# Kernel tuning notes

Measured on AMD Instinct MI355X. Metric: run time of the kernel, lower is better.

## Reference

```python
import jax, jax.numpy as jnp
import numpy as np

NUM_HEADS = 16
D_MODEL = 1024
ROPE_THETA = 10000.0


def rope_cos_sin(H, W, head_dim, theta):
    # SAM2/SAM3 axial RoPE: first half of complex dims encode x, second half y.
    n = H * W
    t = jnp.arange(n)
    tx = (t % W).astype(jnp.float32)
    ty = (t // W).astype(jnp.float32)
    # freqs: 1 / theta^(arange(0, dim, 4)[:dim//4] / dim)
    exps = jnp.arange(0, head_dim, 4)[: head_dim // 4].astype(jnp.float32) / head_dim
    freqs = 1.0 / (theta ** exps)  # (head_dim//4,)
    ang = jnp.concatenate([tx[:, None] * freqs, ty[:, None] * freqs], axis=-1)  # (N, head_dim//2)
    return jnp.cos(ang), jnp.sin(ang)


def apply_rope(x, cos, sin):
    # x: (B, nh, N, D); pairs of features treated as complex numbers
    B, nh, N, D = x.shape
    xr = x.reshape(B, nh, N, D // 2, 2)
    xe, xo = xr[..., 0], xr[..., 1]
    oe = xe * cos - xo * sin
    oo = xe * sin + xo * cos
    return jnp.stack([oe, oo], axis=-1).reshape(B, nh, N, D)


def setup_inputs() -> dict:
    key = jax.random.key(0)
    ks = jax.random.split(key, 12)
    C = D_MODEL
    s = 1.0 / np.sqrt(C)
    inp = {
        "q": jax.random.normal(ks[0], (2, 2048, C), dtype=jnp.float32),
        "k": jax.random.normal(ks[1], (2, 2112, C), dtype=jnp.float32),
        "v": jax.random.normal(ks[2], (2, 2112, C), dtype=jnp.float32),
        "Wq": jax.random.normal(ks[3], (C, C), dtype=jnp.float32) * s,
        "bq": jax.random.normal(ks[4], (C,), dtype=jnp.float32) * s,
        "Wk": jax.random.normal(ks[5], (C, C), dtype=jnp.float32) * s,
        "bk": jax.random.normal(ks[6], (C,), dtype=jnp.float32) * s,
        "Wv": jax.random.normal(ks[7], (C, C), dtype=jnp.float32) * s,
        "bv": jax.random.normal(ks[8], (C,), dtype=jnp.float32) * s,
        "Wo": jax.random.normal(ks[9], (C, C), dtype=jnp.float32) * s,
        "bo": jax.random.normal(ks[10], (C,), dtype=jnp.float32) * s,
        "q_h": 32,
        "q_w": 64,
        "num_final_k_to_exclude": 64,
    }
    return inp


def reference(q, k, v, Wq, bq, Wk, bk, Wv, bv, Wo, bo, q_h, q_w, num_final_k_to_exclude):
    B, Nq, C = q.shape
    Nk = k.shape[1]
    nh = NUM_HEADS
    d = C // nh
    # QKV projections -> (B, nh, N, d)
    qh = (q @ Wq + bq).reshape(B, Nq, nh, d).transpose(0, 2, 1, 3)
    kh = (k @ Wk + bk).reshape(B, Nk, nh, d).transpose(0, 2, 1, 3)
    vh = (v @ Wv + bv).reshape(B, Nk, nh, d).transpose(0, 2, 1, 3)
    # RoPE on q and on first num_k_keep keys (exclude trailing pointer tokens)
    n_keep = Nk - num_final_k_to_exclude  # == q_h * q_w == Nq here
    cos, sin = rope_cos_sin(q_h, q_w, d, ROPE_THETA)
    qh = apply_rope(qh, cos, sin)
    k_rot = apply_rope(kh[:, :, :n_keep], cos, sin)
    kh = jnp.concatenate([k_rot, kh[:, :, n_keep:]], axis=2)
    # scaled dot-product attention
    scale = 1.0 / np.sqrt(d)
    scores = jnp.einsum("bhqd,bhkd->bhqk", qh, kh) * scale
    probs = jax.nn.softmax(scores, axis=-1)
    attn = jnp.einsum("bhqk,bhkd->bhqd", probs, vh)
    out = attn.transpose(0, 2, 1, 3).reshape(B, Nq, C)
    return out @ Wo + bo
```

## Files before the change

### kernel.cpp

```cpp
#include <hip/hip_runtime.h>

#define B_ 2
#define NQ 2048
#define NK 2112
#define CD 1024
#define NH 16
#define HD 64

typedef unsigned short u16;
typedef unsigned int u32;
typedef __attribute__((ext_vector_type(8))) __bf16 bf16x8;
typedef __attribute__((ext_vector_type(4))) float f32x4;

#define GPTR(p) ((const __attribute__((address_space(1))) void*)(p))
#define LPTR(p) ((__attribute__((address_space(3))) void*)(p))
#define GLL16(g, l) __builtin_amdgcn_global_load_lds(GPTR(g), LPTR(l), 16, 0, 0)

__device__ __forceinline__ u16 f2bf(float f) {
  u32 u = __float_as_uint(f);
  u32 r = u + 0x7fffu + ((u >> 16) & 1u);
  return (u16)(r >> 16);
}
__device__ __forceinline__ u32 pack2bf(float x, float y) {
  u32 a = __float_as_uint(x); a += 0x7fffu + ((a >> 16) & 1u);
  u32 b = __float_as_uint(y); b += 0x7fffu + ((b >> 16) & 1u);
  return __builtin_amdgcn_perm(b, a, 0x07060302u);
}

#define SC 0.18033688011112042f
#define NEGL2T 0.8304820237f
#define FSTEP 0.5623413252f

__global__ void prep_kernel(const float* __restrict__ q, const float* __restrict__ k,
                            const float* __restrict__ v, u16* __restrict__ qb,
                            u16* __restrict__ kb, u16* __restrict__ vb,
                            const float* __restrict__ W0, const float* __restrict__ W1,
                            const float* __restrict__ W2, const float* __restrict__ W3,
                            u16* __restrict__ T0, u16* __restrict__ T1,
                            u16* __restrict__ T2, u16* __restrict__ T3) {
  __shared__ u16 tile[32][33];
  int y = blockIdx.y;
  int t = threadIdx.x;
  if (y < 3) {
    const float* src = (y == 0) ? q : (y == 1) ? k : v;
    u16* dst = (y == 0) ? qb : (y == 1) ? kb : vb;
    int n4 = (y == 0) ? (B_ * NQ * CD / 4) : (B_ * NK * CD / 4);
    int i = blockIdx.x * 256 + t;
    if (i >= n4) return;
    float4 vv = ((const float4*)src)[i];
    ushort4 o;
    o.x = f2bf(vv.x); o.y = f2bf(vv.y); o.z = f2bf(vv.z); o.w = f2bf(vv.w);
    ((ushort4*)dst)[i] = o;
  } else {
    int x = blockIdx.x;
    if (x >= 4096) return;
    int which = x >> 10, xy = x & 1023;
    const float* src = (which == 0) ? W0 : (which == 1) ? W1 : (which == 2) ? W2 : W3;
    u16* dst = (which == 0) ? T0 : (which == 1) ? T1 : (which == 2) ? T2 : T3;
    int r0 = (xy >> 5) * 32, c0 = (xy & 31) * 32;
    int row = t >> 3, c4 = (t & 7) * 4;
    float4 vv = *(const float4*)&src[(r0 + row) * 1024 + c0 + c4];
    tile[row][c4 + 0] = f2bf(vv.x);
    tile[row][c4 + 1] = f2bf(vv.y);
    tile[row][c4 + 2] = f2bf(vv.z);
    tile[row][c4 + 3] = f2bf(vv.w);
    __syncthreads();
    ushort4 o;
    o.x = tile[c4 + 0][row];
    o.y = tile[c4 + 1][row];
    o.z = tile[c4 + 2][row];
    o.w = tile[c4 + 3][row];
    *(ushort4*)&dst[(c0 + row) * 1024 + r0 + c4] = o;
  }
}

__global__ __launch_bounds__(256, 2) void gemm_qkv(
    const u16* __restrict__ qb, const u16* __restrict__ kb, const u16* __restrict__ vb,
    const u16* __restrict__ wqt, const u16* __restrict__ wkt, const u16* __restrict__ wvt,
    const float* __restrict__ bq, const float* __restrict__ bk, const float* __restrict__ bv,
    u16* __restrict__ Qh, u16* __restrict__ Kh, u16* __restrict__ Vt) {
  __shared__ u16 As[2][128 * 32];
  __shared__ u16 Bs[2][128 * 32];
  const int z = blockIdx.z;
  if (z == 0 && blockIdx.y >= 32) return;
  const u16* A = (z == 0) ? qb : (z == 1) ? kb : vb;
  const u16* Bt = (z == 0) ? wqt : (z == 1) ? wkt : wvt;
  const float* bias = (z == 0) ? bq : (z == 1) ? bk : bv;
  const int BR = (z == 0) ? NQ : NK;

  const int t = threadIdx.x;
  const int lane = t & 63, w = t >> 6;
  const int lc = lane & 15, lq = lane >> 4;
  const int m0 = blockIdx.y * 128, n0 = blockIdx.x * 128;
  const int wm = (w >> 1) * 64, wn = (w & 1) * 64;
  f32x4 acc[4][4] = {};
  const u16* ga = A + (m0 + (t >> 2)) * 1024 + (t & 3) * 8;
  const u16* gb = Bt + (n0 + (t >> 2)) * 1024 + (t & 3) * 8;
  char* lA0 = (char*)&As[0][0] + w * 1024;
  char* lA1 = (char*)&As[1][0] + w * 1024;
  char* lB0 = (char*)&Bs[0][0] + w * 1024;
  char* lB1 = (char*)&Bs[1][0] + w * 1024;
  const bool swap = (z < 2);
  for (int k0 = 0; k0 < 1024; k0 += 64) {
    if (k0) __syncthreads();
    GLL16(ga + k0, lA0);
    GLL16(ga + 64 * 1024 + k0, lA0 + 4096);
    GLL16(ga + k0 + 32, lA1);
    GLL16(ga + 64 * 1024 + k0 + 32, lA1 + 4096);
    GLL16(gb + k0, lB0);
    GLL16(gb + 64 * 1024 + k0, lB0 + 4096);
    GLL16(gb + k0 + 32, lB1);
    GLL16(gb + 64 * 1024 + k0 + 32, lB1 + 4096);
    __syncthreads();
#pragma unroll
    for (int kk = 0; kk < 2; ++kk) {
      bf16x8 af[4], bf[4];
#pragma unroll
      for (int i = 0; i < 4; ++i) {
        af[i] = *(const bf16x8*)&As[kk][(wm + i * 16 + lc) * 32 + lq * 8];
        bf[i] = *(const bf16x8*)&Bs[kk][(wn + i * 16 + lc) * 32 + lq * 8];
      }
      if (swap) {
#pragma unroll
        for (int mi = 0; mi < 4; ++mi)
#pragma unroll
          for (int ni = 0; ni < 4; ++ni)
            acc[mi][ni] = __builtin_amdgcn_mfma_f32_16x16x32_bf16(bf[ni], af[mi], acc[mi][ni], 0, 0, 0);
      } else {
#pragma unroll
        for (int mi = 0; mi < 4; ++mi)
#pragma unroll
          for (int ni = 0; ni < 4; ++ni)
            acc[mi][ni] = __builtin_amdgcn_mfma_f32_16x16x32_bf16(af[mi], bf[ni], acc[mi][ni], 0, 0, 0);
      }
    }
  }

  if (swap) {
    u16* Out = (z == 0) ? Qh : Kh;
    const bool isQ = (z == 0);
#pragma unroll
    for (int ni = 0; ni < 4; ++ni) {
      int cb = n0 + wn + ni * 16 + lq * 4;
      float4 bv4 = *(const float4*)&bias[cb];
      int jj = (ni * 8 + lq * 2) & 15;
      bool jl = ni < 2;
      float f0 = exp2f((float)jj * -NEGL2T);
      float f1 = f0 * FSTEP;
#pragma unroll
      for (int mi = 0; mi < 4; ++mi) {
        int row = m0 + wm + mi * 16 + lc;
        int bb = row >= BR ? 1 : 0;
        int tok = row - bb * BR;
        float v0 = acc[mi][ni][0] + bv4.x;
        float v1 = acc[mi][ni][1] + bv4.y;
        float v2 = acc[mi][ni][2] + bv4.z;
        float v3 = acc[mi][ni][3] + bv4.w;
        uint2 pk;
        if (isQ || tok < 2048) {
          float pos = jl ? (float)(tok & 63) : (float)(tok >> 6);
          float s0, c0, s1, c1;
          __sincosf(pos * f0, &s0, &c0);
          __sincosf(pos * f1, &s1, &c1);
          float o0 = v0 * c0 - v1 * s0, o1 = v0 * s0 + v1 * c0;
          float o2 = v2 * c1 - v3 * s1, o3 = v2 * s1 + v3 * c1;
          if (isQ) { o0 *= SC; o1 *= SC; o2 *= SC; o3 *= SC; }
          pk.x = pack2bf(o0, o1);
          pk.y = pack2bf(o2, o3);
        } else {
          pk.x = pack2bf(v0, v1);
          pk.y = pack2bf(v2, v3);
        }
        *(uint2*)&Out[row * 1024 + cb] = pk;
      }
    }
  } else {
#pragma unroll
    for (int ni = 0; ni < 4; ++ni) {
      int col = n0 + wn + ni * 16 + lc;
      float bv = bias[col];
      int hh = col >> 6, dd = col & 63;
#pragma unroll
      for (int mi = 0; mi < 4; ++mi) {
        int row0 = m0 + wm + mi * 16 + lq * 4;
        int bb = row0 >= NK ? 1 : 0;
        int tok0 = row0 - bb * NK;
        uint2 pk;
        pk.x = pack2bf(acc[mi][ni][0] + bv, acc[mi][ni][1] + bv);
        pk.y = pack2bf(acc[mi][ni][2] + bv, acc[mi][ni][3] + bv);
        *(uint2*)&Vt[((bb * NH + hh) * HD + dd) * NK + tok0] = pk;
      }
    }
  }
}

__global__ __launch_bounds__(256, 2) void gemm_o(const u16* __restrict__ A,
                                                 const u16* __restrict__ Bt,
                                                 const float* __restrict__ bias,
                                                 float* __restrict__ Cout) {
  __shared__ u16 As[2][128 * 32];
  __shared__ u16 Bs[2][64 * 32];
  const int t = threadIdx.x;
  const int lane = t & 63, w = t >> 6;
  const int lc = lane & 15, lq = lane >> 4;
  const int m0 = blockIdx.y * 128, n0 = blockIdx.x * 64;
  const int wm = (w >> 1) * 64, wn = (w & 1) * 32;
  f32x4 acc[4][2] = {};
  const u16* ga = A + (m0 + (t >> 2)) * 1024 + (t & 3) * 8;
  const u16* gb = Bt + (n0 + (t >> 2)) * 1024 + (t & 3) * 8;
  char* lA0 = (char*)&As[0][0] + w * 1024;
  char* lA1 = (char*)&As[1][0] + w * 1024;
  char* lB0 = (char*)&Bs[0][0] + w * 1024;
  char* lB1 = (char*)&Bs[1][0] + w * 1024;
  for (int k0 = 0; k0 < 1024; k0 += 64) {
    if (k0) __syncthreads();
    GLL16(ga + k0, lA0);
    GLL16(ga + 64 * 1024 + k0, lA0 + 4096);
    GLL16(ga + k0 + 32, lA1);
    GLL16(ga + 64 * 1024 + k0 + 32, lA1 + 4096);
    GLL16(gb + k0, lB0);
    GLL16(gb + k0 + 32, lB1);
    __syncthreads();
#pragma unroll
    for (int kk = 0; kk < 2; ++kk) {
      bf16x8 af[4], bf[2];
#pragma unroll
      for (int i = 0; i < 4; ++i)
        af[i] = *(const bf16x8*)&As[kk][(wm + i * 16 + lc) * 32 + lq * 8];
#pragma unroll
      for (int i = 0; i < 2; ++i)
        bf[i] = *(const bf16x8*)&Bs[kk][(wn + i * 16 + lc) * 32 + lq * 8];
#pragma unroll
      for (int mi = 0; mi < 4; ++mi)
#pragma unroll
        for (int ni = 0; ni < 2; ++ni)
          acc[mi][ni] = __builtin_amdgcn_mfma_f32_16x16x32_bf16(bf[ni], af[mi], acc[mi][ni], 0, 0, 0);
    }
  }
#pragma unroll
  for (int ni = 0; ni < 2; ++ni) {
    int cb = n0 + wn + ni * 16 + lq * 4;
    float4 bv4 = *(const float4*)&bias[cb];
#pragma unroll
    for (int mi = 0; mi < 4; ++mi) {
      int row = m0 + wm + mi * 16 + lc;
      float4 o;
      o.x = acc[mi][ni][0] + bv4.x;
      o.y = acc[mi][ni][1] + bv4.y;
      o.z = acc[mi][ni][2] + bv4.z;
      o.w = acc[mi][ni][3] + bv4.w;
      *(float4*)&Cout[row * 1024 + cb] = o;
    }
  }
}

#define LSTR 72
__global__ __launch_bounds__(256, 2) void attn_kernel(const u16* __restrict__ Qh,
                                                      const u16* __restrict__ Kh,
                                                      const u16* __restrict__ Vt,
                                                      u16* __restrict__ AO) {
  __shared__ u16 QPs[128 * LSTR];
  __shared__ u16 Ks[2 * 64 * LSTR];
  __shared__ u16 Vs[2 * 64 * LSTR];
  const int t = threadIdx.x;
  const int lane = t & 63, w = t >> 6;
  const int lc = lane & 15, lq = lane >> 4;
  const int rr = lane >> 3, s = lane & 7;
  const int qt = blockIdx.x, h = blockIdx.y, b = blockIdx.z;

  {
    const u16* gq = Qh + (b * NQ + qt * 128 + w * 32 + rr) * CD + h * HD + s * 8;
    u16* lqp = &QPs[(w * 32 + rr) * LSTR + s * 8];
#pragma unroll
    for (int i = 0; i < 4; ++i)
      *(uint4*)(lqp + i * 8 * LSTR) = *(const uint4*)(gq + i * 8 * CD);
  }
  bf16x8 qf[2][2];
#pragma unroll
  for (int ni = 0; ni < 2; ++ni)
#pragma unroll
    for (int kk = 0; kk < 2; ++kk)
      qf[ni][kk] = *(const bf16x8*)&QPs[(w * 32 + ni * 16 + lc) * LSTR + kk * 32 + lq * 8];

  bf16x8 ones;
  {
    u32* op = (u32*)&ones;
    op[0] = op[1] = op[2] = op[3] = 0x3F803F80u;
  }

  const u16* gK = Kh + (b * NK + w * 16 + rr) * CD + h * HD + s * 8;
  const u16* gV = Vt + ((b * NH + h) * HD + w * 16 + rr) * NK + s * 8;
  const int sk0 = (w * 16 + rr) * LSTR + s * 8;
  const int sk1 = (w * 16 + 8 + rr) * LSTR + s * 8;

  uint4 kreg0 = *(const uint4*)(gK);
  uint4 kreg1 = *(const uint4*)(gK + 8 * CD);
  uint4 vreg0 = *(const uint4*)(gV);
  uint4 vreg1 = *(const uint4*)(gV + 8 * NK);
  *(uint4*)&Ks[sk0] = kreg0;
  *(uint4*)&Ks[sk1] = kreg1;
  *(uint4*)&Vs[sk0] = vreg0;
  *(uint4*)&Vs[sk1] = vreg1;
  kreg0 = *(const uint4*)(gK + 64 * CD);
  kreg1 = *(const uint4*)(gK + 64 * CD + 8 * CD);
  vreg0 = *(const uint4*)(gV + 64);
  vreg1 = *(const uint4*)(gV + 8 * NK + 64);
  __syncthreads();

  f32x4 oacc[2][4] = {};
  f32x4 lacc[2] = {};
  int p = 0;

  for (int j0 = 0; j0 < NK; j0 += 64) {
    const u16* Kc = &Ks[p * 64 * LSTR];

    f32x4 st[2][4] = {};
#pragma unroll
    for (int mi = 0; mi < 4; ++mi) {
      bf16x8 k0f = *(const bf16x8*)&Kc[(mi * 16 + lc) * LSTR + lq * 8];
      bf16x8 k1f = *(const bf16x8*)&Kc[(mi * 16 + lc) * LSTR + 32 + lq * 8];
#pragma unroll
      for (int ni = 0; ni < 2; ++ni) {
        st[ni][mi] = __builtin_amdgcn_mfma_f32_16x16x32_bf16(k0f, qf[ni][0], st[ni][mi], 0, 0, 0);
        st[ni][mi] = __builtin_amdgcn_mfma_f32_16x16x32_bf16(k1f, qf[ni][1], st[ni][mi], 0, 0, 0);
      }
    }
#pragma unroll
    for (int ni = 0; ni < 2; ++ni)
#pragma unroll
      for (int mi = 0; mi < 4; ++mi) {
        u32 e0 = __float_as_uint(__builtin_amdgcn_exp2f(st[ni][mi][0]));
        u32 e1 = __float_as_uint(__builtin_amdgcn_exp2f(st[ni][mi][1]));
        u32 e2 = __float_as_uint(__builtin_amdgcn_exp2f(st[ni][mi][2]));
        u32 e3 = __float_as_uint(__builtin_amdgcn_exp2f(st[ni][mi][3]));
        uint2 pk;
        pk.x = __builtin_amdgcn_perm(e1 + 0x8000u, e0 + 0x8000u, 0x07060302u);
        pk.y = __builtin_amdgcn_perm(e3 + 0x8000u, e2 + 0x8000u, 0x07060302u);
        *(uint2*)&QPs[(w * 32 + ni * 16 + lc) * LSTR + mi * 16 + lq * 4] = pk;
      }
#pragma unroll
    for (int kc = 0; kc < 2; ++kc) {
      bf16x8 pf[2], vf[4];
#pragma unroll
      for (int ni = 0; ni < 2; ++ni)
        pf[ni] = *(const bf16x8*)&QPs[(w * 32 + ni * 16 + lc) * LSTR + kc * 32 + lq * 8];
#pragma unroll
      for (int di = 0; di < 4; ++di)
        vf[di] = *(const bf16x8*)&Vs[p * 64 * LSTR + (di * 16 + lc) * LSTR + kc * 32 + lq * 8];
#pragma unroll
      for (int ni = 0; ni < 2; ++ni) {
#pragma unroll
        for (int di = 0; di < 4; ++di)
          oacc[ni][di] = __builtin_amdgcn_mfma_f32_16x16x32_bf16(pf[ni], vf[di], oacc[ni][di], 0, 0, 0);
        lacc[ni] = __builtin_amdgcn_mfma_f32_16x16x32_bf16(pf[ni], ones, lacc[ni], 0, 0, 0);
      }
    }

    if (j0 + 64 < NK) {
      u16* Kn = &Ks[(p ^ 1) * 64 * LSTR];
      u16* Vn = &Vs[(p ^ 1) * 64 * LSTR];
      *(uint4*)&Kn[sk0] = kreg0;
      *(uint4*)&Kn[sk1] = kreg1;
      *(uint4*)&Vn[sk0] = vreg0;
      *(uint4*)&Vn[sk1] = vreg1;
      if (j0 + 128 < NK) {
        kreg0 = *(const uint4*)(gK + (j0 + 128) * CD);
        kreg1 = *(const uint4*)(gK + (j0 + 128) * CD + 8 * CD);
        vreg0 = *(const uint4*)(gV + j0 + 128);
        vreg1 = *(const uint4*)(gV + 8 * NK + j0 + 128);
      }
    }
    __syncthreads();
    p ^= 1;
  }
#pragma unroll
  for (int ni = 0; ni < 2; ++ni)
#pragma unroll
    for (int r = 0; r < 4; ++r) {
      float inv = 1.0f / lacc[ni][r];
#pragma unroll
      for (int di = 0; di < 4; ++di) {
        int row = qt * 128 + w * 32 + ni * 16 + lq * 4 + r;
        int col = h * HD + di * 16 + lc;
        AO[(b * NQ + row) * CD + col] = f2bf(oacc[ni][di][r] * inv);
      }
    }
}

extern "C" void kernel_launch(void* const* d_in, const int* in_sizes, int n_in,
                              void* d_out, int out_size, void* d_ws, size_t ws_size,
                              hipStream_t stream) {
  const float* q  = (const float*)d_in[0];
  const float* k  = (const float*)d_in[1];
  const float* v  = (const float*)d_in[2];
  const float* Wq = (const float*)d_in[3];
  const float* bq = (const float*)d_in[4];
  const float* Wk = (const float*)d_in[5];
  const float* bk = (const float*)d_in[6];
  const float* Wv = (const float*)d_in[7];
  const float* bv = (const float*)d_in[8];
  const float* Wo = (const float*)d_in[9];
  const float* bo = (const float*)d_in[10];

  char* ws = (char*)d_ws;
  size_t off = 0;
  auto alloc = [&](size_t bytes) {
    char* p = ws + off;
    off += (bytes + 255) & ~(size_t)255;
    return p;
  };
  u16* qb  = (u16*)alloc((size_t)B_ * NQ * CD * 2);
  u16* kb  = (u16*)alloc((size_t)B_ * NK * CD * 2);
  u16* vb  = (u16*)alloc((size_t)B_ * NK * CD * 2);
  u16* wqt = (u16*)alloc((size_t)CD * CD * 2);
  u16* wkt = (u16*)alloc((size_t)CD * CD * 2);
  u16* wvt = (u16*)alloc((size_t)CD * CD * 2);
  u16* wot = (u16*)alloc((size_t)CD * CD * 2);
  u16* Qh  = (u16*)alloc((size_t)B_ * NQ * CD * 2);
  u16* Kh  = (u16*)alloc((size_t)B_ * NK * CD * 2);
  u16* Vt  = (u16*)alloc((size_t)B_ * NK * CD * 2);
  u16* AO  = (u16*)alloc((size_t)B_ * NQ * CD * 2);

  prep_kernel<<<dim3(4224, 4), 256, 0, stream>>>(q, k, v, qb, kb, vb,
                                                 Wq, Wk, Wv, Wo, wqt, wkt, wvt, wot);
  gemm_qkv<<<dim3(8, 33, 3), 256, 0, stream>>>(qb, kb, vb, wqt, wkt, wvt, bq, bk, bv, Qh, Kh, Vt);
  attn_kernel<<<dim3(16, NH, B_), 256, 0, stream>>>(Qh, Kh, Vt, AO);
  gemm_o<<<dim3(16, 32), 256, 0, stream>>>(AO, wot, bo, (float*)d_out);
}
```

Baseline: 246.6 us.

## Use 8 waves per attention block and reshape output GEMM tiles

```diff
diff --git a/kernel.cpp b/kernel.cpp
--- a/kernel.cpp
+++ b/kernel.cpp
@@ -194,18 +194,18 @@
   }
 }
 
-__global__ __launch_bounds__(256, 2) void gemm_o(const u16* __restrict__ A,
+__global__ __launch_bounds__(256, 4) void gemm_o(const u16* __restrict__ A,
                                                  const u16* __restrict__ Bt,
                                                  const float* __restrict__ bias,
                                                  float* __restrict__ Cout) {
-  __shared__ u16 As[2][128 * 32];
-  __shared__ u16 Bs[2][64 * 32];
+  __shared__ u16 As[2][64 * 32];
+  __shared__ u16 Bs[2][128 * 32];
   const int t = threadIdx.x;
   const int lane = t & 63, w = t >> 6;
   const int lc = lane & 15, lq = lane >> 4;
-  const int m0 = blockIdx.y * 128, n0 = blockIdx.x * 64;
-  const int wm = (w >> 1) * 64, wn = (w & 1) * 32;
-  f32x4 acc[4][2] = {};
+  const int m0 = blockIdx.y * 64, n0 = blockIdx.x * 128;
+  const int wm = (w >> 1) * 32, wn = (w & 1) * 64;
+  f32x4 acc[2][4] = {};
   const u16* ga = A + (m0 + (t >> 2)) * 1024 + (t & 3) * 8;
   const u16* gb = Bt + (n0 + (t >> 2)) * 1024 + (t & 3) * 8;
   char* lA0 = (char*)&As[0][0] + w * 1024;
@@ -215,34 +215,34 @@
   for (int k0 = 0; k0 < 1024; k0 += 64) {
     if (k0) __syncthreads();
     GLL16(ga + k0, lA0);
-    GLL16(ga + 64 * 1024 + k0, lA0 + 4096);
     GLL16(ga + k0 + 32, lA1);
-    GLL16(ga + 64 * 1024 + k0 + 32, lA1 + 4096);
     GLL16(gb + k0, lB0);
+    GLL16(gb + 64 * 1024 + k0, lB0 + 4096);
     GLL16(gb + k0 + 32, lB1);
+    GLL16(gb + 64 * 1024 + k0 + 32, lB1 + 4096);
     __syncthreads();
 #pragma unroll
     for (int kk = 0; kk < 2; ++kk) {
-      bf16x8 af[4], bf[2];
+      bf16x8 af[2], bf[4];
+#pragma unroll
+      for (int i = 0; i < 2; ++i)
+        af[i] = *(const bf16x8*)&As[kk][(wm + i * 16 + lc) * 32 + lq * 8];
 #pragma unroll
       for (int i = 0; i < 4; ++i)
-        af[i] = *(const bf16x8*)&As[kk][(wm + i * 16 + lc) * 32 + lq * 8];
-#pragma unroll
-      for (int i = 0; i < 2; ++i)
         bf[i] = *(const bf16x8*)&Bs[kk][(wn + i * 16 + lc) * 32 + lq * 8];
 #pragma unroll
-      for (int mi = 0; mi < 4; ++mi)
-#pragma unroll
-        for (int ni = 0; ni < 2; ++ni)
+      for (int mi = 0; mi < 2; ++mi)
+#pragma unroll
+        for (int ni = 0; ni < 4; ++ni)
           acc[mi][ni] = __builtin_amdgcn_mfma_f32_16x16x32_bf16(bf[ni], af[mi], acc[mi][ni], 0, 0, 0);
     }
   }
 #pragma unroll
-  for (int ni = 0; ni < 2; ++ni) {
+  for (int ni = 0; ni < 4; ++ni) {
     int cb = n0 + wn + ni * 16 + lq * 4;
     float4 bv4 = *(const float4*)&bias[cb];
 #pragma unroll
-    for (int mi = 0; mi < 4; ++mi) {
+    for (int mi = 0; mi < 2; ++mi) {
       int row = m0 + wm + mi * 16 + lc;
       float4 o;
       o.x = acc[mi][ni][0] + bv4.x;
@@ -255,7 +255,7 @@
 }
 
 #define LSTR 72
-__global__ __launch_bounds__(256, 2) void attn_kernel(const u16* __restrict__ Qh,
+__global__ __launch_bounds__(512, 4) void attn_kernel(const u16* __restrict__ Qh,
                                                       const u16* __restrict__ Kh,
                                                       const u16* __restrict__ Vt,
                                                       u16* __restrict__ AO) {
@@ -269,18 +269,15 @@
   const int qt = blockIdx.x, h = blockIdx.y, b = blockIdx.z;
 
   {
-    const u16* gq = Qh + (b * NQ + qt * 128 + w * 32 + rr) * CD + h * HD + s * 8;
-    u16* lqp = &QPs[(w * 32 + rr) * LSTR + s * 8];
-#pragma unroll
-    for (int i = 0; i < 4; ++i)
-      *(uint4*)(lqp + i * 8 * LSTR) = *(const uint4*)(gq + i * 8 * CD);
-  }
-  bf16x8 qf[2][2];
-#pragma unroll
-  for (int ni = 0; ni < 2; ++ni)
-#pragma unroll
-    for (int kk = 0; kk < 2; ++kk)
-      qf[ni][kk] = *(const bf16x8*)&QPs[(w * 32 + ni * 16 + lc) * LSTR + kk * 32 + lq * 8];
+    const u16* gq = Qh + (b * NQ + qt * 128 + w * 16 + rr) * CD + h * HD + s * 8;
+    u16* lqp = &QPs[(w * 16 + rr) * LSTR + s * 8];
+    *(uint4*)(lqp) = *(const uint4*)(gq);
+    *(uint4*)(lqp + 8 * LSTR) = *(const uint4*)(gq + 8 * CD);
+  }
+  bf16x8 qf[2];
+#pragma unroll
+  for (int kk = 0; kk < 2; ++kk)
+    qf[kk] = *(const bf16x8*)&QPs[(w * 16 + lc) * LSTR + kk * 32 + lq * 8];
 
   bf16x8 ones;
   {
@@ -288,103 +285,79 @@
     op[0] = op[1] = op[2] = op[3] = 0x3F803F80u;
   }
 
-  const u16* gK = Kh + (b * NK + w * 16 + rr) * CD + h * HD + s * 8;
-  const u16* gV = Vt + ((b * NH + h) * HD + w * 16 + rr) * NK + s * 8;
-  const int sk0 = (w * 16 + rr) * LSTR + s * 8;
-  const int sk1 = (w * 16 + 8 + rr) * LSTR + s * 8;
-
-  uint4 kreg0 = *(const uint4*)(gK);
-  uint4 kreg1 = *(const uint4*)(gK + 8 * CD);
-  uint4 vreg0 = *(const uint4*)(gV);
-  uint4 vreg1 = *(const uint4*)(gV + 8 * NK);
-  *(uint4*)&Ks[sk0] = kreg0;
-  *(uint4*)&Ks[sk1] = kreg1;
-  *(uint4*)&Vs[sk0] = vreg0;
-  *(uint4*)&Vs[sk1] = vreg1;
-  kreg0 = *(const uint4*)(gK + 64 * CD);
-  kreg1 = *(const uint4*)(gK + 64 * CD + 8 * CD);
-  vreg0 = *(const uint4*)(gV + 64);
-  vreg1 = *(const uint4*)(gV + 8 * NK + 64);
+  const u16* gK = Kh + (b * NK + w * 8 + rr) * CD + h * HD + s * 8;
+  const u16* gV = Vt + ((b * NH + h) * HD + w * 8 + rr) * NK + s * 8;
+  const int sk = (w * 8 + rr) * LSTR + s * 8;
+
+  uint4 kreg = *(const uint4*)(gK);
+  uint4 vreg = *(const uint4*)(gV);
+  *(uint4*)&Ks[sk] = kreg;
+  *(uint4*)&Vs[sk] = vreg;
+  kreg = *(const uint4*)(gK + 64 * CD);
+  vreg = *(const uint4*)(gV + 64);
   __syncthreads();
 
-  f32x4 oacc[2][4] = {};
-  f32x4 lacc[2] = {};
+  f32x4 oacc[4] = {};
+  f32x4 lacc = {};
   int p = 0;
 
   for (int j0 = 0; j0 < NK; j0 += 64) {
     const u16* Kc = &Ks[p * 64 * LSTR];
-
-    f32x4 st[2][4] = {};
+    const u16* Vc = &Vs[p * 64 * LSTR];
+
+    f32x4 st[4] = {};
 #pragma unroll
     for (int mi = 0; mi < 4; ++mi) {
       bf16x8 k0f = *(const bf16x8*)&Kc[(mi * 16 + lc) * LSTR + lq * 8];
       bf16x8 k1f = *(const bf16x8*)&Kc[(mi * 16 + lc) * LSTR + 32 + lq * 8];
-#pragma unroll
-      for (int ni = 0; ni < 2; ++ni) {
-        st[ni][mi] = __builtin_amdgcn_mfma_f32_16x16x32_bf16(k0f, qf[ni][0], st[ni][mi], 0, 0, 0);
-        st[ni][mi] = __builtin_amdgcn_mfma_f32_16x16x32_bf16(k1f, qf[ni][1], st[ni][mi], 0, 0, 0);
-      }
-    }
-#pragma unroll
-    for (int ni = 0; ni < 2; ++ni)
-#pragma unroll
-      for (int mi = 0; mi < 4; ++mi) {
-        u32 e0 = __float_as_uint(__builtin_amdgcn_exp2f(st[ni][mi][0]));
-        u32 e1 = __float_as_uint(__builtin_amdgcn_exp2f(st[ni][mi][1]));
-        u32 e2 = __float_as_uint(__builtin_amdgcn_exp2f(st[ni][mi][2]));
-        u32 e3 = __float_as_uint(__builtin_amdgcn_exp2f(st[ni][mi][3]));
-        uint2 pk;
-        pk.x = __builtin_amdgcn_perm(e1 + 0x8000u, e0 + 0x8000u, 0x07060302u);
-        pk.y = __builtin_amdgcn_perm(e3 + 0x8000u, e2 + 0x8000u, 0x07060302u);
-        *(uint2*)&QPs[(w * 32 + ni * 16 + lc) * LSTR + mi * 16 + lq * 4] = pk;
-      }
+      st[mi] = __builtin_amdgcn_mfma_f32_16x16x32_bf16(k0f, qf[0], st[mi], 0, 0, 0);
+      st[mi] = __builtin_amdgcn_mfma_f32_16x16x32_bf16(k1f, qf[1], st[mi], 0, 0, 0);
+    }
+#pragma unroll
+    for (int mi = 0; mi < 4; ++mi) {
+      u32 e0 = __float_as_uint(__builtin_amdgcn_exp2f(st[mi][0]));
+      u32 e1 = __float_as_uint(__builtin_amdgcn_exp2f(st[mi][1]));
+      u32 e2 = __float_as_uint(__builtin_amdgcn_exp2f(st[mi][2]));
+      u32 e3 = __float_as_uint(__builtin_amdgcn_exp2f(st[mi][3]));
+      uint2 pk;
+      pk.x = __builtin_amdgcn_perm(e1 + 0x8000u, e0 + 0x8000u, 0x07060302u);
+      pk.y = __builtin_amdgcn_perm(e3 + 0x8000u, e2 + 0x8000u, 0x07060302u);
+      *(uint2*)&QPs[(w * 16 + lc) * LSTR + mi * 16 + lq * 4] = pk;
+    }
 #pragma unroll
     for (int kc = 0; kc < 2; ++kc) {
-      bf16x8 pf[2], vf[4];
-#pragma unroll
-      for (int ni = 0; ni < 2; ++ni)
-        pf[ni] = *(const bf16x8*)&QPs[(w * 32 + ni * 16 + lc) * LSTR + kc * 32 + lq * 8];
+      bf16x8 pf = *(const bf16x8*)&QPs[(w * 16 + lc) * LSTR + kc * 32 + lq * 8];
+      bf16x8 vf[4];
 #pragma unroll
       for (int di = 0; di < 4; ++di)
-        vf[di] = *(const bf16x8*)&Vs[p * 64 * LSTR + (di * 16 + lc) * LSTR + kc * 32 + lq * 8];
-#pragma unroll
-      for (int ni = 0; ni < 2; ++ni) {
-#pragma unroll
-        for (int di = 0; di < 4; ++di)
-          oacc[ni][di] = __builtin_amdgcn_mfma_f32_16x16x32_bf16(pf[ni], vf[di], oacc[ni][di], 0, 0, 0);
-        lacc[ni] = __builtin_amdgcn_mfma_f32_16x16x32_bf16(pf[ni], ones, lacc[ni], 0, 0, 0);
-      }
+        vf[di] = *(const bf16x8*)&Vc[(di * 16 + lc) * LSTR + kc * 32 + lq * 8];
+#pragma unroll
+      for (int di = 0; di < 4; ++di)
+        oacc[di] = __builtin_amdgcn_mfma_f32_16x16x32_bf16(pf, vf[di], oacc[di], 0, 0, 0);
+      lacc = __builtin_amdgcn_mfma_f32_16x16x32_bf16(pf, ones, lacc, 0, 0, 0);
     }
 
     if (j0 + 64 < NK) {
-      u16* Kn = &Ks[(p ^ 1) * 64 * LSTR];
-      u16* Vn = &Vs[(p ^ 1) * 64 * LSTR];
-      *(uint4*)&Kn[sk0] = kreg0;
-      *(uint4*)&Kn[sk1] = kreg1;
-      *(uint4*)&Vn[sk0] = vreg0;
-      *(uint4*)&Vn[sk1] = vreg1;
+      *(uint4*)&Ks[(p ^ 1) * 64 * LSTR + sk] = kreg;
+      *(uint4*)&Vs[(p ^ 1) * 64 * LSTR + sk] = vreg;
       if (j0 + 128 < NK) {
-        kreg0 = *(const uint4*)(gK + (j0 + 128) * CD);
-        kreg1 = *(const uint4*)(gK + (j0 + 128) * CD + 8 * CD);
-        vreg0 = *(const uint4*)(gV + j0 + 128);
-        vreg1 = *(const uint4*)(gV + 8 * NK + j0 + 128);
+        kreg = *(const uint4*)(gK + (j0 + 128) * CD);
+        vreg = *(const uint4*)(gV + j0 + 128);
       }
     }
     __syncthreads();
     p ^= 1;
   }
 #pragma unroll
-  for (int ni = 0; ni < 2; ++ni)
-#pragma unroll
-    for (int r = 0; r < 4; ++r) {
-      float inv = 1.0f / lacc[ni][r];
-#pragma unroll
-      for (int di = 0; di < 4; ++di) {
-        int row = qt * 128 + w * 32 + ni * 16 + lq * 4 + r;
-        int col = h * HD + di * 16 + lc;
-        AO[(b * NQ + row) * CD + col] = f2bf(oacc[ni][di][r] * inv);
-      }
-    }
+  for (int r = 0; r < 4; ++r) {
+    float inv = 1.0f / lacc[r];
+#pragma unroll
+    for (int di = 0; di < 4; ++di) {
+      int row = qt * 128 + w * 16 + lq * 4 + r;
+      int col = h * HD + di * 16 + lc;
+      AO[(b * NQ + row) * CD + col] = f2bf(oacc[di][r] * inv);
+    }
+  }
 }
 
 extern "C" void kernel_launch(void* const* d_in, const int* in_sizes, int n_in,
@@ -424,6 +397,6 @@
   prep_kernel<<<dim3(4224, 4), 256, 0, stream>>>(q, k, v, qb, kb, vb,
                                                  Wq, Wk, Wv, Wo, wqt, wkt, wvt, wot);
   gemm_qkv<<<dim3(8, 33, 3), 256, 0, stream>>>(qb, kb, vb, wqt, wkt, wvt, bq, bk, bv, Qh, Kh, Vt);
-  attn_kernel<<<dim3(16, NH, B_), 256, 0, stream>>>(Qh, Kh, Vt, AO);
-  gemm_o<<<dim3(16, 32), 256, 0, stream>>>(AO, wot, bo, (float*)d_out);
-}
+  attn_kernel<<<dim3(16, NH, B_), 512, 0, stream>>>(Qh, Kh, Vt, AO);
+  gemm_o<<<dim3(8, 64), 256, 0, stream>>>(AO, wot, bo, (float*)d_out);
+}
```

Measured after the change: 251.0 us. Within noise of the previous version (+1.8%).
